# Optimization experiments

Measured on AMD Instinct MI355X. Metric: run time of the kernel, lower is better.

The kernel has to match this reference:

```python
import jax, jax.numpy as jnp
import numpy as np

N_NODES = 100000
N_EDGES = 600000
NODE_DIM = 64
EDGE_DIM = 32
HID = 128
OUT = 24


def setup_inputs() -> dict:
    key = jax.random.key(0)
    ks = jax.random.split(key, 20)

    def w(k, shape):
        return jax.random.normal(k, shape, jnp.float32) * (1.0 / np.sqrt(shape[0]).astype(np.float32))

    inp = {}
    inp["x"] = jax.random.normal(ks[0], (N_NODES, NODE_DIM), jnp.float32)
    inp["edge_index"] = jax.random.randint(ks[1], (2, N_EDGES), 0, N_NODES)
    inp["edge_attr"] = jax.random.normal(ks[2], (N_EDGES, EDGE_DIM), jnp.float32)
    inp["lin1_w"] = w(ks[3], (NODE_DIM, HID)); inp["lin1_b"] = jnp.zeros((HID,), jnp.float32)
    i = 4
    for c in (1, 2, 3):
        inp[f"conv{c}_edge_w"] = w(ks[i], (EDGE_DIM, HID)); inp[f"conv{c}_edge_b"] = jnp.zeros((HID,), jnp.float32)
        inp[f"conv{c}_w1"] = w(ks[i + 1], (HID, HID)); inp[f"conv{c}_b1"] = jnp.zeros((HID,), jnp.float32)
        inp[f"conv{c}_w2"] = w(ks[i + 2], (HID, HID)); inp[f"conv{c}_b2"] = jnp.zeros((HID,), jnp.float32)
        i += 3
    inp["cls_w1"] = w(ks[i], (2 * HID + EDGE_DIM, HID)); inp["cls_b1"] = jnp.zeros((HID,), jnp.float32)
    inp["cls_w2"] = w(ks[i + 1], (HID, OUT)); inp["cls_b2"] = jnp.zeros((OUT,), jnp.float32)
    return inp


def _gine(h, src, dst, e_emb, w1, b1, w2, b2, eps=0.0):
    # GINEConv: out = MLP((1+eps)*x + sum_{j->i} relu(x_j + edge_emb))
    m = jax.nn.relu(h[src] + e_emb)                       # [E, HID] gather + fuse
    agg = jax.ops.segment_sum(m, dst, num_segments=N_NODES)  # scatter-add to dst
    z = (1.0 + eps) * h + agg
    return jax.nn.relu(z @ w1 + b1) @ w2 + b2


def reference(x, edge_index, edge_attr,
              lin1_w, lin1_b,
              conv1_edge_w, conv1_edge_b, conv1_w1, conv1_b1, conv1_w2, conv1_b2,
              conv2_edge_w, conv2_edge_b, conv2_w1, conv2_b1, conv2_w2, conv2_b2,
              conv3_edge_w, conv3_edge_b, conv3_w1, conv3_b1, conv3_w2, conv3_b2,
              cls_w1, cls_b1, cls_w2, cls_b2):
    src, dst = edge_index[0], edge_index[1]
    h = x @ lin1_w + lin1_b                               # [N, HID]
    layers = [
        (conv1_edge_w, conv1_edge_b, conv1_w1, conv1_b1, conv1_w2, conv1_b2),
        (conv2_edge_w, conv2_edge_b, conv2_w1, conv2_b1, conv2_w2, conv2_b2),
        (conv3_edge_w, conv3_edge_b, conv3_w1, conv3_b1, conv3_w2, conv3_b2),
    ]
    for ew, eb, w1, b1, w2, b2 in layers:
        e_emb = edge_attr @ ew + eb                       # [E, HID]
        h = jax.nn.relu(_gine(h, src, dst, e_emb, w1, b1, w2, b2))
    edge_feat = jnp.concatenate([h[src], h[dst], edge_attr], axis=-1)  # [E, 2*HID+EDGE_DIM]
    return jax.nn.relu(edge_feat @ cls_w1 + cls_b1) @ cls_w2 + cls_b2  # [E, OUT]
```

## Files before the change

### kernel.cpp

```cpp
#include <hip/hip_runtime.h>

#define N_NODES 100000
#define N_EDGES 600000
#define NODE_DIM 64
#define EDGE_DIM 32
#define HID 128
#define OUT_DIM 24

typedef short short8 __attribute__((ext_vector_type(8)));
typedef short short4v __attribute__((ext_vector_type(4)));
typedef float f32x4 __attribute__((ext_vector_type(4)));

#define MFMA16(a, b, c) __builtin_amdgcn_mfma_f32_16x16x32_bf16(a, b, c, 0, 0, 0)

__device__ inline unsigned short f2bf(float f) {
  unsigned u = __float_as_uint(f);
  u += 0x7FFFu + ((u >> 16) & 1u);
  return (unsigned short)(u >> 16);
}
__device__ inline float bf2f(unsigned short b) {
  return __uint_as_float(((unsigned)b) << 16);
}

#define OFF_CW1T 0
#define OFF_CW2T 36864
#define OFF_LAYER(c) (40960 + (c)*65536)
#define OFF_EWT(c) (237568 + (c)*8192)
#define W_TOTAL 262144

__global__ __launch_bounds__(256) void prep_weights(
    const float* __restrict__ cw1, const float* __restrict__ cw2,
    const float* __restrict__ l0w1, const float* __restrict__ l0w2,
    const float* __restrict__ l1w1, const float* __restrict__ l1w2,
    const float* __restrict__ l2w1, const float* __restrict__ l2w2,
    const float* __restrict__ e0w, const float* __restrict__ e1w,
    const float* __restrict__ e2w,
    unsigned short* __restrict__ wb) {
  int i = blockIdx.x * 256 + threadIdx.x;
  if (i < 36864) {
    int c = i >> 12, v = i & 4095;
    int f = v >> 3, jj = v & 7;
    int t = f >> 6, l = f & 63;
    int n = t * 16 + (l & 15);
    int k = c * 32 + (l >> 4) * 8 + jj;
    wb[OFF_CW1T + i] = f2bf(cw1[k * 128 + n]);
  }
  int j = i - 36864;
  if (j >= 0 && j < 4096) {
    int f = j >> 3, jj = j & 7;
    int nt2 = f >> 8, rem = f & 255;
    int kc = rem >> 6, l = rem & 63;
    int n = nt2 * 16 + (l & 15);
    int k = kc * 32 + (l >> 4) * 8 + jj;
    wb[OFF_CW2T + j] = f2bf(n < 24 ? cw2[k * 24 + n] : 0.f);
  }
  int t = i - 40960;
  if (t >= 0 && t < 3 * 32768) {
    int c = t / 32768, u = t % 32768;
    const float* w = (u < 16384) ? (c == 0 ? l0w1 : c == 1 ? l1w1 : l2w1)
                                 : (c == 0 ? l0w2 : c == 1 ? l1w2 : l2w2);
    int v = u & 16383;
    int n = v >> 7, k = v & 127;
    float val = w[k * 128 + n];
    unsigned short hi = f2bf(val);
    unsigned short lo = f2bf(val - bf2f(hi));
    int base = OFF_LAYER(c) + (u < 16384 ? 0 : 32768);
    wb[base + v] = hi;
    wb[base + 16384 + v] = lo;
  }
  int p = i - 139264;
  if (p >= 0 && p < 3 * 8192) {
    int c = p / 8192, u = p % 8192;
    int v = u & 4095;
    int s = v >> 3, jj = v & 7;
    int ntile = s >> 6, kgrp = (s >> 4) & 3, nrow = s & 15;
    int n = ntile * 16 + nrow, k = kgrp * 8 + jj;
    const float* ew = (c == 0 ? e0w : c == 1 ? e1w : e2w);
    float val = ew[k * 128 + n];
    unsigned short hi = f2bf(val);
    wb[OFF_EWT(c) + u] = (u < 4096) ? hi : f2bf(val - bf2f(hi));
  }
}

__global__ __launch_bounds__(256) void lin1_kernel(
    const float* __restrict__ x, const float* __restrict__ w,
    const float* __restrict__ b, float* __restrict__ h,
    unsigned short* __restrict__ hbf) {
  __shared__ float4 smem4[3072];
  float* sA = (float*)smem4;
  float* sB = (float*)smem4 + 4096;
  int tid = threadIdx.x;
  int tn = tid & 31, tm = tid >> 5;
  int mbase = blockIdx.x * 64;

  for (int i = tid; i < 1024; i += 256) {
    int m = i & 63, k4 = (i >> 6) << 2;
    int row = mbase + m; if (row >= N_NODES) row = N_NODES - 1;
    float4 v = *(const float4*)(x + (size_t)row * NODE_DIM + k4);
    sA[(k4 + 0) * 64 + m] = v.x; sA[(k4 + 1) * 64 + m] = v.y;
    sA[(k4 + 2) * 64 + m] = v.z; sA[(k4 + 3) * 64 + m] = v.w;
  }
  for (int i = tid; i < 2048; i += 256)
    *(float4*)&sB[i * 4] = ((const float4*)w)[i];
  __syncthreads();

  float acc[8][4] = {};
#pragma unroll 8
  for (int k = 0; k < 64; ++k) {
    float4 a0 = *(float4*)&sA[k * 64 + tm * 8];
    float4 a1 = *(float4*)&sA[k * 64 + tm * 8 + 4];
    float4 bv = *(float4*)&sB[k * 128 + tn * 4];
    float av[8] = {a0.x, a0.y, a0.z, a0.w, a1.x, a1.y, a1.z, a1.w};
    float bb[4] = {bv.x, bv.y, bv.z, bv.w};
#pragma unroll
    for (int i = 0; i < 8; ++i)
#pragma unroll
      for (int jj = 0; jj < 4; ++jj) acc[i][jj] = fmaf(av[i], bb[jj], acc[i][jj]);
  }
  float4 bv = *(const float4*)(b + tn * 4);
#pragma unroll
  for (int i = 0; i < 8; ++i) {
    int row = mbase + tm * 8 + i;
    if (row < N_NODES) {
      float4 o = {acc[i][0] + bv.x, acc[i][1] + bv.y, acc[i][2] + bv.z, acc[i][3] + bv.w};
      *(float4*)(h + (size_t)row * HID + tn * 4) = o;
      short4v pk = {(short)f2bf(o.x), (short)f2bf(o.y), (short)f2bf(o.z), (short)f2bf(o.w)};
      *(short4v*)(hbf + (size_t)row * HID + tn * 4) = pk;
    }
  }
}

__global__ __launch_bounds__(256) void hist_kernel(
    const int* __restrict__ dst, int* __restrict__ counts) {
  int e = blockIdx.x * 256 + threadIdx.x;
  if (e < N_EDGES) atomicAdd(&counts[dst[e]], 1);
}

#define SCAN_BLK 98
__global__ __launch_bounds__(256) void scan_partial(
    const int* __restrict__ cnt, int* __restrict__ partial) {
  __shared__ int sdata[256];
  int b = blockIdx.x, t = threadIdx.x;
  int sum = 0;
  for (int i = t; i < 1024; i += 256) {
    int idx = b * 1024 + i;
    sum += (idx < N_NODES) ? cnt[idx] : 0;
  }
  sdata[t] = sum; __syncthreads();
  for (int s = 128; s > 0; s >>= 1) {
    if (t < s) sdata[t] += sdata[t + s];
    __syncthreads();
  }
  if (t == 0) partial[b] = sdata[0];
}

__global__ void scan_sums(const int* __restrict__ partial,
                          int* __restrict__ partialScan, int* __restrict__ rowptr) {
  if (threadIdx.x == 0) {
    int acc = 0;
    for (int i = 0; i < SCAN_BLK; ++i) { partialScan[i] = acc; acc += partial[i]; }
    rowptr[N_NODES] = acc;
  }
}

__global__ __launch_bounds__(256) void scan_final(
    const int* __restrict__ cnt, const int* __restrict__ partialScan,
    int* __restrict__ rowptr, int* __restrict__ cur) {
  __shared__ int sdata[256];
  int b = blockIdx.x, t = threadIdx.x;
  int i0 = b * 1024 + t * 4;
  int c[4]; int s = 0;
#pragma unroll
  for (int j = 0; j < 4; ++j) {
    c[j] = (i0 + j < N_NODES) ? cnt[i0 + j] : 0;
    s += c[j];
  }
  sdata[t] = s; __syncthreads();
  for (int d = 1; d < 256; d <<= 1) {
    int u = (t >= d) ? sdata[t - d] : 0;
    __syncthreads();
    sdata[t] += u;
    __syncthreads();
  }
  int off = sdata[t] - s + partialScan[b];
#pragma unroll
  for (int j = 0; j < 4; ++j) {
    int idx = i0 + j;
    if (idx < N_NODES) { rowptr[idx] = off; cur[idx] = off; off += c[j]; }
  }
}

__global__ __launch_bounds__(256) void scatter_kernel(
    const int* __restrict__ dst, const int* __restrict__ src,
    int* __restrict__ cur, int* __restrict__ perm,
    int* __restrict__ srcp, int* __restrict__ dstp) {
  int e = blockIdx.x * 256 + threadIdx.x;
  if (e < N_EDGES) {
    int d = dst[e];
    int slot = atomicAdd(&cur[d], 1);
    perm[slot] = e;
    srcp[slot] = src[e];
    dstp[slot] = d;
  }
}

__global__ __launch_bounds__(256) void build_eafrag(
    const float* __restrict__ ea, const int* __restrict__ perm,
    unsigned short* __restrict__ frag) {
  int slot = blockIdx.x * 256 + threadIdx.x;
  if (slot >= N_EDGES) return;
  int e = perm[slot];
  const float4* row = (const float4*)(ea + (size_t)e * EDGE_DIM);
  unsigned short* dp = frag + ((size_t)(slot >> 7)) * 4096 +
                       (size_t)(((slot & 127) >> 4)) * 512 + (slot & 15) * 8;
#pragma unroll
  for (int kg = 0; kg < 4; ++kg) {
    float4 v0 = row[kg * 2], v1 = row[kg * 2 + 1];
    short8 pk = {(short)f2bf(v0.x), (short)f2bf(v0.y), (short)f2bf(v0.z), (short)f2bf(v0.w),
                 (short)f2bf(v1.x), (short)f2bf(v1.y), (short)f2bf(v1.z), (short)f2bf(v1.w)};
    *(short8*)(dp + kg * 128) = pk;
  }
}

__global__ __launch_bounds__(256) void edge_agg_kernel(
    const unsigned short* __restrict__ hbf, const unsigned short* __restrict__ eafrag,
    const int* __restrict__ srcp, const int* __restrict__ dstp,
    const unsigned short* __restrict__ ewt, const float* __restrict__ eb,
    float* __restrict__ agg) {
  __shared__ float emb[128 * 132];
  __shared__ int sidx[128];
  __shared__ int sdst[128];
  int tid = threadIdx.x, lane = tid & 63, wave = tid >> 6;
  int wm = wave & 1, wn = wave >> 1;
  int sbase = blockIdx.x * 128;
  int nrows = N_EDGES - sbase; if (nrows > 128) nrows = 128;
  if (tid < 128) {
    int sl = sbase + tid;
    sidx[tid] = (sl < N_EDGES) ? srcp[sl] : 0;
    sdst[tid] = (sl < N_EDGES) ? dstp[sl] : -1;
  }
  __syncthreads();

  int r0 = wave * 32;
  int cl = (lane & 31) * 4;
  uint2 g[16];
#pragma unroll
  for (int rr = 0; rr < 16; ++rr) {
    int row = r0 + rr * 2 + (lane >> 5);
    g[rr] = *(const uint2*)(hbf + (size_t)sidx[row] * HID + cl);
  }

  const short8* Af = (const short8*)(eafrag) + (size_t)blockIdx.x * 512;
  const short8* Bh = (const short8*)(ewt);
  const short8* Bl = (const short8*)(ewt + 4096);
  short8 af[4], bh[4], bl[4];
#pragma unroll
  for (int mt = 0; mt < 4; ++mt) af[mt] = Af[(wm * 4 + mt) * 64 + lane];
#pragma unroll
  for (int nt = 0; nt < 4; ++nt) {
    bh[nt] = Bh[(wn * 4 + nt) * 64 + lane];
    bl[nt] = Bl[(wn * 4 + nt) * 64 + lane];
  }
  const f32x4 zf = {0.f, 0.f, 0.f, 0.f};
  f32x4 acc[4][4];
#pragma unroll
  for (int mt = 0; mt < 4; ++mt)
#pragma unroll
    for (int nt = 0; nt < 4; ++nt) {
      acc[mt][nt] = MFMA16(af[mt], bh[nt], zf);
      acc[mt][nt] = MFMA16(af[mt], bl[nt], acc[mt][nt]);
    }
  int q = lane >> 4, r = lane & 15;
#pragma unroll
  for (int nt = 0; nt < 4; ++nt) {
    int n = wn * 64 + nt * 16 + r;
    float ebv = eb[n];
#pragma unroll
    for (int mt = 0; mt < 4; ++mt) {
      int rowb = (wm * 4 + mt) * 16 + q * 4;
#pragma unroll
      for (int i2 = 0; i2 < 4; ++i2)
        emb[(rowb + i2) * 132 + n] = acc[mt][nt][i2] + ebv;
    }
  }
  __syncthreads();
#pragma unroll
  for (int rr = 0; rr < 16; ++rr) {
    int row = r0 + rr * 2 + (lane >> 5);
    float4 ev = *(float4*)(emb + row * 132 + cl);
    uint2 u = g[rr];
    ev.x = fmaxf(ev.x + bf2f((unsigned short)u.x), 0.f);
    ev.y = fmaxf(ev.y + bf2f((unsigned short)(u.x >> 16)), 0.f);
    ev.z = fmaxf(ev.z + bf2f((unsigned short)u.y), 0.f);
    ev.w = fmaxf(ev.w + bf2f((unsigned short)(u.y >> 16)), 0.f);
    *(float4*)(emb + row * 132 + cl) = ev;
  }
  __syncthreads();
  {
    int hh = tid >> 7;
    int col = tid & 127;
    int rbeg = hh * 64;
    int rend = rbeg + 64; if (rend > nrows) rend = nrows;
    if (rbeg < rend) {
      float a = 0.f;
      int cnode = sdst[rbeg];
      bool atomic_first = true;
      for (int rr = rbeg; rr < rend; ++rr) {
        int node = sdst[rr];
        if (node != cnode) {
          if (atomic_first) atomicAdd(&agg[(size_t)cnode * HID + col], a);
          else agg[(size_t)cnode * HID + col] = a;
          a = 0.f; cnode = node; atomic_first = false;
        }
        a += emb[rr * 132 + col];
      }
      atomicAdd(&agg[(size_t)cnode * HID + col], a);
    }
  }
}

__global__ __launch_bounds__(256) void agg_gather_kernel(
    const float* __restrict__ h, const float* __restrict__ ea,
    const int* __restrict__ srcp, const int* __restrict__ perm,
    const int* __restrict__ rowptr,
    const float* __restrict__ ew, const float* __restrict__ eb,
    float* __restrict__ agg) {
  int tid = threadIdx.x, lane = tid & 63;
  int wid = blockIdx.x * 4 + (tid >> 6);
  int nwaves = gridDim.x * 4;
  const float2* ew2 = (const float2*)ew;
  float2 ebv = *(const float2*)(eb + lane * 2);

  for (int node = wid; node < N_NODES; node += nwaves) {
    int beg = rowptr[node], end = rowptr[node + 1];
    float2 acc = {0.f, 0.f};
    for (int i = beg; i < end; ++i) {
      int s0 = srcp[i];
      int e0 = perm[i];
      float2 h0 = *(const float2*)(h + (size_t)s0 * HID + lane * 2);
      const float4* ea0 = (const float4*)(ea + (size_t)e0 * EDGE_DIM);
      float2 m0 = ebv;
#pragma unroll
      for (int k4 = 0; k4 < 8; ++k4) {
        float4 a0 = ea0[k4];
        float a0v[4] = {a0.x, a0.y, a0.z, a0.w};
#pragma unroll
        for (int j = 0; j < 4; ++j) {
          float2 w = ew2[(k4 * 4 + j) * 64 + lane];
          m0.x = fmaf(a0v[j], w.x, m0.x);
          m0.y = fmaf(a0v[j], w.y, m0.y);
        }
      }
      acc.x += fmaxf(m0.x + h0.x, 0.f);
      acc.y += fmaxf(m0.y + h0.y, 0.f);
    }
    *(float2*)(agg + (size_t)node * HID + lane * 2) = acc;
  }
}

__global__ __launch_bounds__(256) void mlp_mfma(
    const float* __restrict__ h, const float* __restrict__ agg,
    const unsigned short* __restrict__ wl,
    const float* __restrict__ b1, const float* __restrict__ b2,
    float* __restrict__ hout, unsigned short* __restrict__ hbfout) {
  __shared__ unsigned short lds[40960];
  unsigned short* sAh = lds;
  unsigned short* sAl = lds + 4096;
  unsigned short* sBh = lds + 8192;
  unsigned short* sBl = lds + 12288;
  unsigned short* t1h = lds;
  unsigned short* t1l = lds + 16384;
  unsigned short* sB2h = lds + 32768;
  unsigned short* sB2l = lds + 36864;
  const unsigned short* w1h = wl;
  const unsigned short* w1l = wl + 16384;
  const unsigned short* w2h = wl + 32768;
  const unsigned short* w2l = wl + 49152;
  int tid = threadIdx.x, lane = tid & 63, wave = tid >> 6;
  int wm = wave & 1, wn = wave >> 1;
  int mbase = blockIdx.x * 128;
  const f32x4 zf = {0.f, 0.f, 0.f, 0.f};

  f32x4 acc[4][4];
#pragma unroll
  for (int a = 0; a < 4; ++a)
#pragma unroll
    for (int bq = 0; bq < 4; ++bq) acc[a][bq] = zf;

  for (int c = 0; c < 4; ++c) {
    __syncthreads();
#pragma unroll
    for (int it = 0; it < 4; ++it) {
      int idx = it * 256 + tid;
      int m = idx >> 3, k4 = (idx & 7) * 4;
      int row = mbase + m; if (row >= N_NODES) row = N_NODES - 1;
      size_t g = (size_t)row * HID + c * 32 + k4;
      float4 hv = *(const float4*)(h + g);
      float4 av = *(const float4*)(agg + g);
      float z0 = hv.x + av.x, z1 = hv.y + av.y, z2 = hv.z + av.z, z3 = hv.w + av.w;
      unsigned short h0 = f2bf(z0), h1 = f2bf(z1), h2 = f2bf(z2), h3 = f2bf(z3);
      int slot = ((m >> 4) * 4 + (k4 >> 3)) * 16 + (m & 15);
      int off = slot * 8 + (k4 & 7);
      short4v ph = {(short)h0, (short)h1, (short)h2, (short)h3};
      short4v pl = {(short)f2bf(z0 - bf2f(h0)), (short)f2bf(z1 - bf2f(h1)),
                    (short)f2bf(z2 - bf2f(h2)), (short)f2bf(z3 - bf2f(h3))};
      *(short4v*)(sAh + off) = ph;
      *(short4v*)(sAl + off) = pl;
    }
#pragma unroll
    for (int it = 0; it < 2; ++it) {
      int s = it * 256 + tid;
      int ntile = s >> 6, kgrp = (s >> 4) & 3, nrow = s & 15;
      int goff = (ntile * 16 + nrow) * 128 + c * 32 + kgrp * 8;
      *(short8*)(sBh + s * 8) = *(const short8*)(w1h + goff);
      *(short8*)(sBl + s * 8) = *(const short8*)(w1l + goff);
    }
    __syncthreads();
    short8 ah[4], al[4], bh[4], bl[4];
#pragma unroll
    for (int mt = 0; mt < 4; ++mt) {
      ah[mt] = *(short8*)(sAh + ((wm * 4 + mt) * 64 + lane) * 8);
      al[mt] = *(short8*)(sAl + ((wm * 4 + mt) * 64 + lane) * 8);
    }
#pragma unroll
    for (int nt = 0; nt < 4; ++nt) {
      bh[nt] = *(short8*)(sBh + ((wn * 4 + nt) * 64 + lane) * 8);
      bl[nt] = *(short8*)(sBl + ((wn * 4 + nt) * 64 + lane) * 8);
    }
#pragma unroll
    for (int mt = 0; mt < 4; ++mt)
#pragma unroll
      for (int nt = 0; nt < 4; ++nt) {
        acc[mt][nt] = MFMA16(ah[mt], bh[nt], acc[mt][nt]);
        acc[mt][nt] = MFMA16(ah[mt], bl[nt], acc[mt][nt]);
        acc[mt][nt] = MFMA16(al[mt], bh[nt], acc[mt][nt]);
      }
  }
  __syncthreads();
  int q = lane >> 4, r = lane & 15;
#pragma unroll
  for (int nt = 0; nt < 4; ++nt) {
    int n = wn * 64 + nt * 16 + r;
    float b1v = b1[n];
    int kgrp = n >> 3, jj = n & 7;
#pragma unroll
    for (int mt = 0; mt < 4; ++mt) {
      int mtg = wm * 4 + mt;
#pragma unroll
      for (int i2 = 0; i2 < 4; ++i2) {
        int mrow = q * 4 + i2;
        float val = fmaxf(acc[mt][nt][i2] + b1v, 0.f);
        unsigned short hi = f2bf(val);
        int idx = ((mtg * 16 + kgrp) * 16 + mrow) * 8 + jj;
        t1h[idx] = hi;
        t1l[idx] = f2bf(val - bf2f(hi));
      }
    }
  }

  f32x4 acc2[4][4];
#pragma unroll
  for (int a = 0; a < 4; ++a)
#pragma unroll
    for (int bq = 0; bq < 4; ++bq) acc2[a][bq] = zf;

  for (int kc = 0; kc < 4; ++kc) {
    __syncthreads();
#pragma unroll
    for (int it = 0; it < 2; ++it) {
      int s = it * 256 + tid;
      int ntile = s >> 6, kgrp = (s >> 4) & 3, nrow = s & 15;
      int goff = (ntile * 16 + nrow) * 128 + kc * 32 + kgrp * 8;
      *(short8*)(sB2h + s * 8) = *(const short8*)(w2h + goff);
      *(short8*)(sB2l + s * 8) = *(const short8*)(w2l + goff);
    }
    __syncthreads();
    short8 ah[4], al[4], bh[4], bl[4];
#pragma unroll
    for (int mt = 0; mt < 4; ++mt) {
      int mtg = wm * 4 + mt;
      int idx = ((mtg * 16 + kc * 4 + q) * 16 + r) * 8;
      ah[mt] = *(short8*)(t1h + idx);
      al[mt] = *(short8*)(t1l + idx);
    }
#pragma unroll
    for (int nt = 0; nt < 4; ++nt) {
      bh[nt] = *(short8*)(sB2h + ((wn * 4 + nt) * 64 + lane) * 8);
      bl[nt] = *(short8*)(sB2l + ((wn * 4 + nt) * 64 + lane) * 8);
    }
#pragma unroll
    for (int mt = 0; mt < 4; ++mt)
#pragma unroll
      for (int nt = 0; nt < 4; ++nt) {
        acc2[mt][nt] = MFMA16(ah[mt], bh[nt], acc2[mt][nt]);
        acc2[mt][nt] = MFMA16(ah[mt], bl[nt], acc2[mt][nt]);
        acc2[mt][nt] = MFMA16(al[mt], bh[nt], acc2[mt][nt]);
      }
  }
#pragma unroll
  for (int nt = 0; nt < 4; ++nt) {
    int n = wn * 64 + nt * 16 + r;
    float b2v = b2[n];
#pragma unroll
    for (int mt = 0; mt < 4; ++mt) {
      int mtg = wm * 4 + mt;
#pragma unroll
      for (int i2 = 0; i2 < 4; ++i2) {
        int row = mbase + mtg * 16 + q * 4 + i2;
        if (row < N_NODES) {
          float val = fmaxf(acc2[mt][nt][i2] + b2v, 0.f);
          hout[(size_t)row * HID + n] = val;
          hbfout[(size_t)row * HID + n] = f2bf(val);
        }
      }
    }
  }
}

__global__ __launch_bounds__(256) void cls_mfma(
    const unsigned short* __restrict__ hbf, const float* __restrict__ ea,
    const int* __restrict__ src, const int* __restrict__ dst,
    const unsigned short* __restrict__ w1f, const unsigned short* __restrict__ w2f,
    const float* __restrict__ b1, const float* __restrict__ b2,
    float* __restrict__ out) {
  __shared__ unsigned short lds[16384];
  unsigned short* t1 = lds;
  __shared__ int sidx[256];
  int tid = threadIdx.x, lane = tid & 63, wave = tid >> 6;
  int wm = wave & 1, wn = wave >> 1;
  int q = lane >> 4, r = lane & 15;
  int ebase = blockIdx.x * 128;
  const f32x4 zf = {0.f, 0.f, 0.f, 0.f};

  {
    int e0 = ebase + (tid & 127);
    if (e0 >= N_EDGES) e0 = N_EDGES - 1;
    sidx[tid] = (tid < 128 ? src : dst)[e0];
  }
  __syncthreads();

  f32x4 acc[4][4];
#pragma unroll
  for (int a = 0; a < 4; ++a)
#pragma unroll
    for (int bq = 0; bq < 4; ++bq) acc[a][bq] = zf;

  int sub = tid & 7, mb = tid >> 3;
  int ch = sub >> 2, kg = sub & 3;

  short8 pf[4];
#pragma unroll
  for (int it = 0; it < 4; ++it) {
    int m = it * 32 + mb;
    pf[it] = *(const short8*)(hbf + (size_t)sidx[m] * HID + sub * 8);
  }
  float4 ef[4];

  for (int cp = 0; cp < 4; ++cp) {
    unsigned short* bufA = lds + (cp & 1) * 8192;
#pragma unroll
    for (int it = 0; it < 4; ++it) {
      int m = it * 32 + mb;
      *(short8*)(bufA + ch * 4096 +
                 (((m >> 4) * 4 + kg) * 16 + ((m & 15) ^ sub)) * 8) = pf[it];
    }
    if (cp < 3) {
      int ncp = cp + 1;
      int eoff = (ncp & 1) * 64;
#pragma unroll
      for (int it = 0; it < 4; ++it) {
        int m = it * 32 + mb;
        int node = (ncp < 2) ? sidx[m] : sidx[128 + m];
        pf[it] = *(const short8*)(hbf + (size_t)node * HID + eoff + sub * 8);
      }
    } else {
#pragma unroll
      for (int it = 0; it < 4; ++it) {
        int m = it * 32 + mb;
        int e8 = ebase + m; if (e8 >= N_EDGES) e8 = N_EDGES - 1;
        ef[it] = *(const float4*)(ea + (size_t)e8 * EDGE_DIM + sub * 4);
      }
    }
    __syncthreads();
#pragma unroll
    for (int ch2 = 0; ch2 < 2; ++ch2) {
      int c = cp * 2 + ch2;
      short8 af[4], bfv[4];
#pragma unroll
      for (int nt = 0; nt < 4; ++nt)
        bfv[nt] = *(const short8*)(w1f + (size_t)c * 4096 + ((wn * 4 + nt) * 64 + lane) * 8);
#pragma unroll
      for (int mt = 0; mt < 4; ++mt)
        af[mt] = *(short8*)(bufA + ch2 * 4096 +
                            (((wm * 4 + mt) * 4 + q) * 16 + (r ^ (ch2 * 4 + q))) * 8);
#pragma unroll
      for (int mt = 0; mt < 4; ++mt)
#pragma unroll
        for (int nt = 0; nt < 4; ++nt)
          acc[mt][nt] = MFMA16(af[mt], bfv[nt], acc[mt][nt]);
    }
  }
  {
    unsigned short* bufA = lds;
    int k4 = sub * 4, kgE = k4 >> 3;
#pragma unroll
    for (int it = 0; it < 4; ++it) {
      int m = it * 32 + mb;
      float4 v = ef[it];
      int slot = ((m >> 4) * 4 + kgE) * 16 + ((m & 15) ^ kgE);
      short4v pk = {(short)f2bf(v.x), (short)f2bf(v.y), (short)f2bf(v.z), (short)f2bf(v.w)};
      *(short4v*)(bufA + slot * 8 + (k4 & 7)) = pk;
    }
    __syncthreads();
    short8 af[4], bfv[4];
#pragma unroll
    for (int nt = 0; nt < 4; ++nt)
      bfv[nt] = *(const short8*)(w1f + (size_t)8 * 4096 + ((wn * 4 + nt) * 64 + lane) * 8);
#pragma unroll
    for (int mt = 0; mt < 4; ++mt)
      af[mt] = *(short8*)(bufA + (((wm * 4 + mt) * 4 + q) * 16 + (r ^ q)) * 8);
#pragma unroll
    for (int mt = 0; mt < 4; ++mt)
#pragma unroll
      for (int nt = 0; nt < 4; ++nt)
        acc[mt][nt] = MFMA16(af[mt], bfv[nt], acc[mt][nt]);
  }
  __syncthreads();
#pragma unroll
  for (int nt = 0; nt < 4; ++nt) {
    int n = wn * 64 + nt * 16 + r;
    float b1v = b1[n];
    int kgrp = n >> 3, jj = n & 7;
#pragma unroll
    for (int mt = 0; mt < 4; ++mt) {
      int mtg = wm * 4 + mt;
#pragma unroll
      for (int i2 = 0; i2 < 4; ++i2) {
        int mrow = q * 4 + i2;
        float val = fmaxf(acc[mt][nt][i2] + b1v, 0.f);
        t1[((mtg * 16 + kgrp) * 16 + mrow) * 8 + jj] = f2bf(val);
      }
    }
  }
  __syncthreads();

  f32x4 acc2[2][2];
  acc2[0][0] = zf; acc2[0][1] = zf; acc2[1][0] = zf; acc2[1][1] = zf;
#pragma unroll
  for (int kc = 0; kc < 4; ++kc) {
    short8 a0 = *(short8*)(t1 + (((wave * 2 + 0) * 16 + kc * 4 + q) * 16 + r) * 8);
    short8 a1 = *(short8*)(t1 + (((wave * 2 + 1) * 16 + kc * 4 + q) * 16 + r) * 8);
    short8 b0 = *(const short8*)(w2f + (kc * 64 + lane) * 8);
    short8 b1f = *(const short8*)(w2f + (256 + kc * 64 + lane) * 8);
    acc2[0][0] = MFMA16(a0, b0, acc2[0][0]);
    acc2[0][1] = MFMA16(a0, b1f, acc2[0][1]);
    acc2[1][0] = MFMA16(a1, b0, acc2[1][0]);
    acc2[1][1] = MFMA16(a1, b1f, acc2[1][1]);
  }
#pragma unroll
  for (int nt2 = 0; nt2 < 2; ++nt2) {
    int n = nt2 * 16 + r;
    float b2v = (n < OUT_DIM) ? b2[n] : 0.f;
#pragma unroll
    for (int mt2 = 0; mt2 < 2; ++mt2) {
      int mtg = wave * 2 + mt2;
#pragma unroll
      for (int i2 = 0; i2 < 4; ++i2) {
        int e = ebase + mtg * 16 + q * 4 + i2;
        if (n < OUT_DIM && e < N_EDGES)
          out[(size_t)e * OUT_DIM + n] = acc2[mt2][nt2][i2] + b2v;
      }
    }
  }
}

extern "C" void kernel_launch(void* const* d_in, const int* in_sizes, int n_in,
                              void* d_out, int out_size, void* d_ws, size_t ws_size,
                              hipStream_t stream) {
  const float* x = (const float*)d_in[0];
  const int* ei = (const int*)d_in[1];
  const float* ea = (const float*)d_in[2];
  const float* lin1_w = (const float*)d_in[3];
  const float* lin1_b = (const float*)d_in[4];
  const int* src = ei;
  const int* dst = ei + N_EDGES;

  const size_t NH = (size_t)N_NODES * HID;
  float* bufA = (float*)d_ws;
  float* bufB = bufA + NH;
  int* ibase = (int*)(bufB + NH);
  int* rowptr = ibase;
  int* cur = ibase + 100004;
  int* counts = ibase + 200004;
  int* perm = ibase + 300004;
  int* partial = ibase + 900004;
  int* partialScan = ibase + 900132;
  int* srcp = ibase + 900260;
  int* dstp = ibase + 1500260;
  unsigned short* hbf = (unsigned short*)(ibase + 2100264);
  unsigned short* eafrag = hbf + (size_t)N_NODES * HID;
  size_t need = (size_t)((char*)(eafrag + (size_t)N_EDGES * EDGE_DIM) - (char*)d_ws) +
                (size_t)W_TOTAL * 2 + 4096;
  bool big = ws_size >= need;
  unsigned short* wbase = (unsigned short*)((((uintptr_t)d_ws + ws_size) - (size_t)W_TOTAL * 2) & ~(uintptr_t)255);

  prep_weights<<<(163840 + 255) / 256, 256, 0, stream>>>(
      (const float*)d_in[23], (const float*)d_in[25],
      (const float*)d_in[7], (const float*)d_in[9],
      (const float*)d_in[13], (const float*)d_in[15],
      (const float*)d_in[19], (const float*)d_in[21],
      (const float*)d_in[5], (const float*)d_in[11], (const float*)d_in[17],
      wbase);

  lin1_kernel<<<(N_NODES + 63) / 64, 256, 0, stream>>>(x, lin1_w, lin1_b, bufA, hbf);

  hipMemsetAsync(counts, 0, N_NODES * sizeof(int), stream);
  hist_kernel<<<(N_EDGES + 255) / 256, 256, 0, stream>>>(dst, counts);
  scan_partial<<<SCAN_BLK, 256, 0, stream>>>(counts, partial);
  scan_sums<<<1, 64, 0, stream>>>(partial, partialScan, rowptr);
  scan_final<<<SCAN_BLK, 256, 0, stream>>>(counts, partialScan, rowptr, cur);
  scatter_kernel<<<(N_EDGES + 255) / 256, 256, 0, stream>>>(dst, src, cur, perm, srcp, dstp);
  if (big)
    build_eafrag<<<(N_EDGES + 255) / 256, 256, 0, stream>>>(ea, perm, eafrag);

  float* hcur = bufA;
  float* aux = bufB;
  for (int c = 0; c < 3; ++c) {
    const float* ew = (const float*)d_in[5 + c * 6 + 0];
    const float* eb = (const float*)d_in[5 + c * 6 + 1];
    const float* b1 = (const float*)d_in[5 + c * 6 + 3];
    const float* b2 = (const float*)d_in[5 + c * 6 + 5];
    if (big) {
      hipMemsetAsync(aux, 0, NH * sizeof(float), stream);
      edge_agg_kernel<<<(N_EDGES + 127) / 128, 256, 0, stream>>>(
          hbf, eafrag, srcp, dstp, wbase + OFF_EWT(c), eb, aux);
    } else {
      agg_gather_kernel<<<2048, 256, 0, stream>>>(
          hcur, ea, srcp, perm, rowptr, ew, eb, aux);
    }
    mlp_mfma<<<(N_NODES + 127) / 128, 256, 0, stream>>>(
        hcur, aux, wbase + OFF_LAYER(c), b1, b2, aux, hbf);
    float* tmp = hcur; hcur = aux; aux = tmp;
  }

  const float* cb1 = (const float*)d_in[24];
  const float* cb2 = (const float*)d_in[26];
  cls_mfma<<<(N_EDGES + 127) / 128, 256, 0, stream>>>(
      hbf, ea, src, dst, wbase + OFF_CW1T, wbase + OFF_CW2T, cb1, cb2, (float*)d_out);
}
```

Baseline: 917.7 us.

## Store edge messages as bf16 in LDS and reuse sorted edge fragments in classifier

The edge aggregation kernel now keeps edge embeddings and messages in LDS as bf16 instead of fp32. This halves LDS footprint, which may allow more resident blocks, at the cost of extra rounding before the sum. The classifier gets a new path that walks edges in dst-sorted order. It reads the pre-converted bf16 edge_attr fragments instead of reconverting fp32 edge_attr, improves gather locality on dst, and scatters its output rows back through the permutation.

After: 901.8 us. No clear change (-1.7%).

```diff
diff --git a/kernel.cpp b/kernel.cpp
--- a/kernel.cpp
+++ b/kernel.cpp
@@ -227,7 +227,7 @@
     const int* __restrict__ srcp, const int* __restrict__ dstp,
     const unsigned short* __restrict__ ewt, const float* __restrict__ eb,
     float* __restrict__ agg) {
-  __shared__ float emb[128 * 132];
+  __shared__ unsigned short emb[128 * 132];
   __shared__ int sidx[128];
   __shared__ int sdst[128];
   int tid = threadIdx.x, lane = tid & 63, wave = tid >> 6;
@@ -280,20 +280,22 @@
       int rowb = (wm * 4 + mt) * 16 + q * 4;
 #pragma unroll
       for (int i2 = 0; i2 < 4; ++i2)
-        emb[(rowb + i2) * 132 + n] = acc[mt][nt][i2] + ebv;
+        emb[(rowb + i2) * 132 + n] = f2bf(acc[mt][nt][i2] + ebv);
     }
   }
   __syncthreads();
 #pragma unroll
   for (int rr = 0; rr < 16; ++rr) {
     int row = r0 + rr * 2 + (lane >> 5);
-    float4 ev = *(float4*)(emb + row * 132 + cl);
+    unsigned* ep = (unsigned*)(emb + row * 132 + cl);
+    unsigned e0 = ep[0], e1 = ep[1];
     uint2 u = g[rr];
-    ev.x = fmaxf(ev.x + bf2f((unsigned short)u.x), 0.f);
-    ev.y = fmaxf(ev.y + bf2f((unsigned short)(u.x >> 16)), 0.f);
-    ev.z = fmaxf(ev.z + bf2f((unsigned short)u.y), 0.f);
-    ev.w = fmaxf(ev.w + bf2f((unsigned short)(u.y >> 16)), 0.f);
-    *(float4*)(emb + row * 132 + cl) = ev;
+    float m0 = fmaxf(bf2f((unsigned short)e0) + bf2f((unsigned short)u.x), 0.f);
+    float m1 = fmaxf(bf2f((unsigned short)(e0 >> 16)) + bf2f((unsigned short)(u.x >> 16)), 0.f);
+    float m2 = fmaxf(bf2f((unsigned short)e1) + bf2f((unsigned short)u.y), 0.f);
+    float m3 = fmaxf(bf2f((unsigned short)(e1 >> 16)) + bf2f((unsigned short)(u.y >> 16)), 0.f);
+    ep[0] = ((unsigned)f2bf(m1) << 16) | f2bf(m0);
+    ep[1] = ((unsigned)f2bf(m3) << 16) | f2bf(m2);
   }
   __syncthreads();
   {
@@ -312,7 +314,7 @@
           else agg[(size_t)cnode * HID + col] = a;
           a = 0.f; cnode = node; atomic_first = false;
         }
-        a += emb[rr * 132 + col];
+        a += bf2f(emb[rr * 132 + col]);
       }
       atomicAdd(&agg[(size_t)cnode * HID + col], a);
     }
@@ -517,7 +519,152 @@
   }
 }
 
-__global__ __launch_bounds__(256) void cls_mfma(
+__global__ __launch_bounds__(256) void cls_mfma_perm(
+    const unsigned short* __restrict__ hbf, const unsigned short* __restrict__ eafrag,
+    const int* __restrict__ srcp, const int* __restrict__ dstp,
+    const int* __restrict__ perm,
+    const unsigned short* __restrict__ w1f, const unsigned short* __restrict__ w2f,
+    const float* __restrict__ b1, const float* __restrict__ b2,
+    float* __restrict__ out) {
+  __shared__ unsigned short lds[16384];
+  unsigned short* t1 = lds;
+  __shared__ int sidx[256];
+  __shared__ int sperm[128];
+  int tid = threadIdx.x, lane = tid & 63, wave = tid >> 6;
+  int wm = wave & 1, wn = wave >> 1;
+  int q = lane >> 4, r = lane & 15;
+  int ebase = blockIdx.x * 128;
+  const f32x4 zf = {0.f, 0.f, 0.f, 0.f};
+
+  {
+    int sl0 = ebase + (tid & 127);
+    if (sl0 >= N_EDGES) sl0 = N_EDGES - 1;
+    sidx[tid] = (tid < 128 ? srcp : dstp)[sl0];
+    if (tid < 128) sperm[tid] = perm[sl0];
+  }
+  __syncthreads();
+
+  const short8* AfE = (const short8*)(eafrag) + (size_t)blockIdx.x * 512;
+  short8 afE[4];
+#pragma unroll
+  for (int mt = 0; mt < 4; ++mt) afE[mt] = AfE[(wm * 4 + mt) * 64 + lane];
+
+  f32x4 acc[4][4];
+#pragma unroll
+  for (int a = 0; a < 4; ++a)
+#pragma unroll
+    for (int bq = 0; bq < 4; ++bq) acc[a][bq] = zf;
+
+  int sub = tid & 7, mb = tid >> 3;
+  int ch = sub >> 2, kg = sub & 3;
+
+  short8 pf[4];
+#pragma unroll
+  for (int it = 0; it < 4; ++it) {
+    int m = it * 32 + mb;
+    pf[it] = *(const short8*)(hbf + (size_t)sidx[m] * HID + sub * 8);
+  }
+
+  for (int cp = 0; cp < 4; ++cp) {
+    unsigned short* bufA = lds + (cp & 1) * 8192;
+#pragma unroll
+    for (int it = 0; it < 4; ++it) {
+      int m = it * 32 + mb;
+      *(short8*)(bufA + ch * 4096 +
+                 (((m >> 4) * 4 + kg) * 16 + ((m & 15) ^ sub)) * 8) = pf[it];
+    }
+    if (cp < 3) {
+      int ncp = cp + 1;
+      int eoff = (ncp & 1) * 64;
+#pragma unroll
+      for (int it = 0; it < 4; ++it) {
+        int m = it * 32 + mb;
+        int node = (ncp < 2) ? sidx[m] : sidx[128 + m];
+        pf[it] = *(const short8*)(hbf + (size_t)node * HID + eoff + sub * 8);
+      }
+    }
+    __syncthreads();
+#pragma unroll
+    for (int ch2 = 0; ch2 < 2; ++ch2) {
+      int c = cp * 2 + ch2;
+      short8 af[4], bfv[4];
+#pragma unroll
+      for (int nt = 0; nt < 4; ++nt)
+        bfv[nt] = *(const short8*)(w1f + (size_t)c * 4096 + ((wn * 4 + nt) * 64 + lane) * 8);
+#pragma unroll
+      for (int mt = 0; mt < 4; ++mt)
+        af[mt] = *(short8*)(bufA + ch2 * 4096 +
+                            (((wm * 4 + mt) * 4 + q) * 16 + (r ^ (ch2 * 4 + q))) * 8);
+#pragma unroll
+      for (int mt = 0; mt < 4; ++mt)
+#pragma unroll
+        for (int nt = 0; nt < 4; ++nt)
+          acc[mt][nt] = MFMA16(af[mt], bfv[nt], acc[mt][nt]);
+    }
+  }
+  {
+    short8 bfv[4];
+#pragma unroll
+    for (int nt = 0; nt < 4; ++nt)
+      bfv[nt] = *(const short8*)(w1f + (size_t)8 * 4096 + ((wn * 4 + nt) * 64 + lane) * 8);
+#pragma unroll
+    for (int mt = 0; mt < 4; ++mt)
+#pragma unroll
+      for (int nt = 0; nt < 4; ++nt)
+        acc[mt][nt] = MFMA16(afE[mt], bfv[nt], acc[mt][nt]);
+  }
+  __syncthreads();
+#pragma unroll
+  for (int nt = 0; nt < 4; ++nt) {
+    int n = wn * 64 + nt * 16 + r;
+    float b1v = b1[n];
+    int kgrp = n >> 3, jj = n & 7;
+#pragma unroll
+    for (int mt = 0; mt < 4; ++mt) {
+      int mtg = wm * 4 + mt;
+#pragma unroll
+      for (int i2 = 0; i2 < 4; ++i2) {
+        int mrow = q * 4 + i2;
+        float val = fmaxf(acc[mt][nt][i2] + b1v, 0.f);
+        t1[((mtg * 16 + kgrp) * 16 + mrow) * 8 + jj] = f2bf(val);
+      }
+    }
+  }
+  __syncthreads();
+
+  f32x4 acc2[2][2];
+  acc2[0][0] = zf; acc2[0][1] = zf; acc2[1][0] = zf; acc2[1][1] = zf;
+#pragma unroll
+  for (int kc = 0; kc < 4; ++kc) {
+    short8 a0 = *(short8*)(t1 + (((wave * 2 + 0) * 16 + kc * 4 + q) * 16 + r) * 8);
+    short8 a1 = *(short8*)(t1 + (((wave * 2 + 1) * 16 + kc * 4 + q) * 16 + r) * 8);
+    short8 b0 = *(const short8*)(w2f + (kc * 64 + lane) * 8);
+    short8 b1f = *(const short8*)(w2f + (256 + kc * 64 + lane) * 8);
+    acc2[0][0] = MFMA16(a0, b0, acc2[0][0]);
+    acc2[0][1] = MFMA16(a0, b1f, acc2[0][1]);
+    acc2[1][0] = MFMA16(a1, b0, acc2[1][0]);
+    acc2[1][1] = MFMA16(a1, b1f, acc2[1][1]);
+  }
+#pragma unroll
+  for (int nt2 = 0; nt2 < 2; ++nt2) {
+    int n = nt2 * 16 + r;
+    float b2v = (n < OUT_DIM) ? b2[n] : 0.f;
+#pragma unroll
+    for (int mt2 = 0; mt2 < 2; ++mt2) {
+      int mtg = wave * 2 + mt2;
+#pragma unroll
+      for (int i2 = 0; i2 < 4; ++i2) {
+        int row = mtg * 16 + q * 4 + i2;
+        if (n < OUT_DIM && ebase + row < N_EDGES) {
+          int e = sperm[row];
+          out[(size_t)e * OUT_DIM + n] = acc2[mt2][nt2][i2] + b2v;
+        }
+      }
+    }
+  }
+}
+
+__global__ __launch_bounds__(256) void cls_mfma_direct(
     const unsigned short* __restrict__ hbf, const float* __restrict__ ea,
     const int* __restrict__ src, const int* __restrict__ dst,
     const unsigned short* __restrict__ w1f, const unsigned short* __restrict__ w2f,
@@ -531,23 +678,19 @@
   int q = lane >> 4, r = lane & 15;
   int ebase = blockIdx.x * 128;
   const f32x4 zf = {0.f, 0.f, 0.f, 0.f};
-
   {
     int e0 = ebase + (tid & 127);
     if (e0 >= N_EDGES) e0 = N_EDGES - 1;
     sidx[tid] = (tid < 128 ? src : dst)[e0];
   }
   __syncthreads();
-
   f32x4 acc[4][4];
 #pragma unroll
   for (int a = 0; a < 4; ++a)
 #pragma unroll
     for (int bq = 0; bq < 4; ++bq) acc[a][bq] = zf;
-
   int sub = tid & 7, mb = tid >> 3;
   int ch = sub >> 2, kg = sub & 3;
-
   short8 pf[4];
 #pragma unroll
   for (int it = 0; it < 4; ++it) {
@@ -555,7 +698,6 @@
     pf[it] = *(const short8*)(hbf + (size_t)sidx[m] * HID + sub * 8);
   }
   float4 ef[4];
-
   for (int cp = 0; cp < 4; ++cp) {
     unsigned short* bufA = lds + (cp & 1) * 8192;
 #pragma unroll
@@ -643,7 +785,6 @@
     }
   }
   __syncthreads();
-
   f32x4 acc2[2][2];
   acc2[0][0] = zf; acc2[0][1] = zf; acc2[1][0] = zf; acc2[1][1] = zf;
 #pragma unroll
@@ -745,6 +886,12 @@
 
   const float* cb1 = (const float*)d_in[24];
   const float* cb2 = (const float*)d_in[26];
-  cls_mfma<<<(N_EDGES + 127) / 128, 256, 0, stream>>>(
-      hbf, ea, src, dst, wbase + OFF_CW1T, wbase + OFF_CW2T, cb1, cb2, (float*)d_out);
-}
+  if (big) {
+    cls_mfma_perm<<<(N_EDGES + 127) / 128, 256, 0, stream>>>(
+        hbf, eafrag, srcp, dstp, perm,
+        wbase + OFF_CW1T, wbase + OFF_CW2T, cb1, cb2, (float*)d_out);
+  } else {
+    cls_mfma_direct<<<(N_EDGES + 127) / 128, 256, 0, stream>>>(
+        hbf, ea, src, dst, wbase + OFF_CW1T, wbase + OFF_CW2T, cb1, cb2, (float*)d_out);
+  }
+}
```

## Prepack MLP weights in MFMA fragment order and store edge messages as bf16 in LDS

Applied to the files above, without the earlier changes.

The weight-prep kernel now writes the layer MLP weights already in MFMA B-fragment order. The MLP kernel loads B fragments straight from global memory instead of staging them through LDS, which removes the LDS weight buffers and several barriers and shrinks shared memory. Separately, the edge aggregation kernel keeps edge embeddings and messages in LDS as bf16 rather than fp32, halving LDS footprint and traffic. That adds rounding error to the summed messages, and the weight loads now depend on cache hits.

New measurement: 864.2 us. 5.8% less time.

```diff
diff --git a/kernel.cpp b/kernel.cpp
--- a/kernel.cpp
+++ b/kernel.cpp
@@ -60,7 +60,10 @@
     const float* w = (u < 16384) ? (c == 0 ? l0w1 : c == 1 ? l1w1 : l2w1)
                                  : (c == 0 ? l0w2 : c == 1 ? l1w2 : l2w2);
     int v = u & 16383;
-    int n = v >> 7, k = v & 127;
+    int kc = v >> 12, f = (v >> 3) & 511, jj = v & 7;
+    int t8 = f >> 6, l = f & 63;
+    int n = t8 * 16 + (l & 15);
+    int k = kc * 32 + (l >> 4) * 8 + jj;
     float val = w[k * 128 + n];
     unsigned short hi = f2bf(val);
     unsigned short lo = f2bf(val - bf2f(hi));
@@ -227,7 +230,7 @@
     const int* __restrict__ srcp, const int* __restrict__ dstp,
     const unsigned short* __restrict__ ewt, const float* __restrict__ eb,
     float* __restrict__ agg) {
-  __shared__ float emb[128 * 132];
+  __shared__ unsigned short emb[128 * 132];
   __shared__ int sidx[128];
   __shared__ int sdst[128];
   int tid = threadIdx.x, lane = tid & 63, wave = tid >> 6;
@@ -280,20 +283,22 @@
       int rowb = (wm * 4 + mt) * 16 + q * 4;
 #pragma unroll
       for (int i2 = 0; i2 < 4; ++i2)
-        emb[(rowb + i2) * 132 + n] = acc[mt][nt][i2] + ebv;
+        emb[(rowb + i2) * 132 + n] = f2bf(acc[mt][nt][i2] + ebv);
     }
   }
   __syncthreads();
 #pragma unroll
   for (int rr = 0; rr < 16; ++rr) {
     int row = r0 + rr * 2 + (lane >> 5);
-    float4 ev = *(float4*)(emb + row * 132 + cl);
+    unsigned* ep = (unsigned*)(emb + row * 132 + cl);
+    unsigned e0 = ep[0], e1 = ep[1];
     uint2 u = g[rr];
-    ev.x = fmaxf(ev.x + bf2f((unsigned short)u.x), 0.f);
-    ev.y = fmaxf(ev.y + bf2f((unsigned short)(u.x >> 16)), 0.f);
-    ev.z = fmaxf(ev.z + bf2f((unsigned short)u.y), 0.f);
-    ev.w = fmaxf(ev.w + bf2f((unsigned short)(u.y >> 16)), 0.f);
-    *(float4*)(emb + row * 132 + cl) = ev;
+    float m0 = fmaxf(bf2f((unsigned short)e0) + bf2f((unsigned short)u.x), 0.f);
+    float m1 = fmaxf(bf2f((unsigned short)(e0 >> 16)) + bf2f((unsigned short)(u.x >> 16)), 0.f);
+    float m2 = fmaxf(bf2f((unsigned short)e1) + bf2f((unsigned short)u.y), 0.f);
+    float m3 = fmaxf(bf2f((unsigned short)(e1 >> 16)) + bf2f((unsigned short)(u.y >> 16)), 0.f);
+    ep[0] = ((unsigned)f2bf(m1) << 16) | f2bf(m0);
+    ep[1] = ((unsigned)f2bf(m3) << 16) | f2bf(m2);
   }
   __syncthreads();
   {
@@ -312,7 +317,7 @@
           else agg[(size_t)cnode * HID + col] = a;
           a = 0.f; cnode = node; atomic_first = false;
         }
-        a += emb[rr * 132 + col];
+        a += bf2f(emb[rr * 132 + col]);
       }
       atomicAdd(&agg[(size_t)cnode * HID + col], a);
     }
@@ -363,15 +368,11 @@
     const unsigned short* __restrict__ wl,
     const float* __restrict__ b1, const float* __restrict__ b2,
     float* __restrict__ hout, unsigned short* __restrict__ hbfout) {
-  __shared__ unsigned short lds[40960];
+  __shared__ unsigned short lds[32768];
   unsigned short* sAh = lds;
   unsigned short* sAl = lds + 4096;
-  unsigned short* sBh = lds + 8192;
-  unsigned short* sBl = lds + 12288;
   unsigned short* t1h = lds;
   unsigned short* t1l = lds + 16384;
-  unsigned short* sB2h = lds + 32768;
-  unsigned short* sB2l = lds + 36864;
   const unsigned short* w1h = wl;
   const unsigned short* w1l = wl + 16384;
   const unsigned short* w2h = wl + 32768;
@@ -407,25 +408,18 @@
       *(short4v*)(sAh + off) = ph;
       *(short4v*)(sAl + off) = pl;
     }
-#pragma unroll
-    for (int it = 0; it < 2; ++it) {
-      int s = it * 256 + tid;
-      int ntile = s >> 6, kgrp = (s >> 4) & 3, nrow = s & 15;
-      int goff = (ntile * 16 + nrow) * 128 + c * 32 + kgrp * 8;
-      *(short8*)(sBh + s * 8) = *(const short8*)(w1h + goff);
-      *(short8*)(sBl + s * 8) = *(const short8*)(w1l + goff);
-    }
     __syncthreads();
     short8 ah[4], al[4], bh[4], bl[4];
+#pragma unroll
+    for (int nt = 0; nt < 4; ++nt) {
+      int fo = c * 4096 + ((wn * 4 + nt) * 64 + lane) * 8;
+      bh[nt] = *(const short8*)(w1h + fo);
+      bl[nt] = *(const short8*)(w1l + fo);
+    }
 #pragma unroll
     for (int mt = 0; mt < 4; ++mt) {
       ah[mt] = *(short8*)(sAh + ((wm * 4 + mt) * 64 + lane) * 8);
       al[mt] = *(short8*)(sAl + ((wm * 4 + mt) * 64 + lane) * 8);
-    }
-#pragma unroll
-    for (int nt = 0; nt < 4; ++nt) {
-      bh[nt] = *(short8*)(sBh + ((wn * 4 + nt) * 64 + lane) * 8);
-      bl[nt] = *(short8*)(sBl + ((wn * 4 + nt) * 64 + lane) * 8);
     }
 #pragma unroll
     for (int mt = 0; mt < 4; ++mt)
@@ -457,6 +451,7 @@
       }
     }
   }
+  __syncthreads();
 
   f32x4 acc2[4][4];
 #pragma unroll
@@ -465,28 +460,19 @@
     for (int bq = 0; bq < 4; ++bq) acc2[a][bq] = zf;
 
   for (int kc = 0; kc < 4; ++kc) {
-    __syncthreads();
-#pragma unroll
-    for (int it = 0; it < 2; ++it) {
-      int s = it * 256 + tid;
-      int ntile = s >> 6, kgrp = (s >> 4) & 3, nrow = s & 15;
-      int goff = (ntile * 16 + nrow) * 128 + kc * 32 + kgrp * 8;
-      *(short8*)(sB2h + s * 8) = *(const short8*)(w2h + goff);
-      *(short8*)(sB2l + s * 8) = *(const short8*)(w2l + goff);
-    }
-    __syncthreads();
     short8 ah[4], al[4], bh[4], bl[4];
+#pragma unroll
+    for (int nt = 0; nt < 4; ++nt) {
+      int fo = kc * 4096 + ((wn * 4 + nt) * 64 + lane) * 8;
+      bh[nt] = *(const short8*)(w2h + fo);
+      bl[nt] = *(const short8*)(w2l + fo);
+    }
 #pragma unroll
     for (int mt = 0; mt < 4; ++mt) {
       int mtg = wm * 4 + mt;
       int idx = ((mtg * 16 + kc * 4 + q) * 16 + r) * 8;
       ah[mt] = *(short8*)(t1h + idx);
       al[mt] = *(short8*)(t1l + idx);
-    }
-#pragma unroll
-    for (int nt = 0; nt < 4; ++nt) {
-      bh[nt] = *(short8*)(sB2h + ((wn * 4 + nt) * 64 + lane) * 8);
-      bl[nt] = *(short8*)(sB2l + ((wn * 4 + nt) * 64 + lane) * 8);
     }
 #pragma unroll
     for (int mt = 0; mt < 4; ++mt)
```
